# Optimization experiments

Hardware: AMD Instinct MI355X
Metric: run time of the kernel (lower is better)

Reference implementation:

```python
import jax, jax.numpy as jnp
import numpy as np

EPS = 1e-6


def ln_fwd(x, gamma, beta):
    # layernorm over last dim (biased variance), per TTT ln_fwd
    mu = x.mean(-1, keepdims=True)
    var = x.var(-1, keepdims=True)
    xh = (x - mu) * jax.lax.rsqrt(var + EPS)
    return gamma * xh + beta


def ln_fused_l2_bwd(x, l2_target, gamma, beta):
    # grad of 0.5*||LN(x) - target||^2 w.r.t. x, fused (per TTT ln_fused_l2_bwd)
    D = x.shape[-1]
    mu = x.mean(-1, keepdims=True)
    var = x.var(-1, keepdims=True)
    std = jnp.sqrt(var + EPS)
    xh = (x - mu) / std
    y = gamma * xh + beta
    gxh = (y - l2_target) * gamma
    z = (D * gxh - gxh.sum(-1, keepdims=True) - xh * (gxh * xh).sum(-1, keepdims=True)) / (D * std)
    return z


def setup_inputs() -> dict:
    key = jax.random.key(0)
    ks = jax.random.split(key, 5)
    B, nh, nmb, mbs, hd = 8, 8, 256, 16, 64
    XQ = jax.random.normal(ks[0], (B, nh, nmb, mbs, hd), jnp.float32)
    XK = jax.random.normal(ks[1], (B, nh, nmb, mbs, hd), jnp.float32)
    XV = jax.random.normal(ks[2], (B, nh, nmb, mbs, hd), jnp.float32)
    # eta = small positive per-token learning rates (ttt_base_lr/head_dim scale)
    eta = jax.random.uniform(ks[3], (B, nh, nmb, mbs, mbs), jnp.float32) * (1.0 / hd)
    W1 = jax.random.normal(ks[4], (nh, hd, hd), jnp.float32) * 0.02
    b1 = jnp.zeros((nh, 1, hd), jnp.float32)
    ln_weight = jnp.ones((nh * hd,), jnp.float32)
    ln_bias = jnp.zeros((nh * hd,), jnp.float32)
    return {"XQ": XQ, "XK": XK, "XV": XV, "eta": eta, "W1": W1, "b1": b1,
            "ln_weight": ln_weight, "ln_bias": ln_bias}


def reference(XQ, XK, XV, eta, W1, b1, ln_weight, ln_bias):
    B, nh, nmb, mbs, hd = XQ.shape
    lnw = ln_weight.reshape(nh, 1, hd)
    lnb = ln_bias.reshape(nh, 1, hd)
    W1_0 = jnp.broadcast_to(W1[None], (B, nh, hd, hd))
    b1_0 = jnp.broadcast_to(b1[None], (B, nh, 1, hd))
    tril = jnp.tril(jnp.ones((mbs, mbs), XQ.dtype))

    def step(carry, inp):
        W1s, b1s = carry               # [B,nh,hd,hd], [B,nh,1,hd]
        xq, xk, xv, et = inp           # [B,nh,mbs,hd] x3, [B,nh,mbs,mbs]
        Z1 = xk @ W1s + b1s
        g = ln_fused_l2_bwd(Z1, xv - xk, lnw, lnb)          # grad_l_wrt_Z1
        Attn1 = tril * (xq @ jnp.swapaxes(xk, -1, -2))      # causal QK^T
        b1_bar = b1s - (tril * et) @ g
        Z1_bar = xq @ W1s - (et * Attn1) @ g + b1_bar
        last_eta = et[..., -1, :, None]                     # [B,nh,mbs,1]
        W1_last = W1s - jnp.swapaxes(last_eta * xk, -1, -2) @ g
        b1_last = b1s - jnp.sum(last_eta * g, axis=-2, keepdims=True)
        out = xq + ln_fwd(Z1_bar, lnw, lnb)
        return (W1_last, b1_last), out

    xs = (jnp.moveaxis(XQ, 2, 0), jnp.moveaxis(XK, 2, 0),
          jnp.moveaxis(XV, 2, 0), jnp.moveaxis(eta, 2, 0))
    _, outs = jax.lax.scan(step, (W1_0, b1_0), xs)
    # outs: [nmb,B,nh,mbs,hd] -> [B,nmb,mbs,nh,hd] -> [B,L,width]
    return jnp.transpose(outs, (1, 0, 3, 2, 4)).reshape(B, nmb * mbs, nh * hd)
```

## Files before the change

kernel.cpp:

```cpp
#include <hip/hip_runtime.h>
#include <hip/hip_bf16.h>

typedef __attribute__((ext_vector_type(8))) short short8;
typedef __attribute__((ext_vector_type(4))) short short4_t;
typedef __attribute__((ext_vector_type(4))) float f32x4;

constexpr int MBS = 16, HD = 64, NMB = 256;

#define MFMA32(a, b, c) __builtin_amdgcn_mfma_f32_16x16x32_bf16(a, b, c, 0, 0, 0)

#if __has_builtin(__builtin_amdgcn_mfma_f32_16x16x16bf16_1k)
#define MFMA16(a, b, c) __builtin_amdgcn_mfma_f32_16x16x16bf16_1k(a, b, c, 0, 0, 0)
#else
__device__ inline f32x4 mfma16_asm(short4_t a, short4_t b, f32x4 c) {
    asm volatile("v_mfma_f32_16x16x16_bf16 %0, %1, %2, %0\n\ts_nop 7\n\ts_nop 7"
                 : "+v"(c) : "v"(a), "v"(b));
    return c;
}
#define MFMA16(a, b, c) mfma16_asm(a, b, c)
#endif

#define TR_READ(dst, addr, IMM) \
    asm volatile("ds_read_b64_tr_b16 %0, %1 offset:" IMM : "=&v"(dst) : "v"(addr) : "memory")

union U2S4 { unsigned u[2]; short4_t s; };
union FI { float f; int i; };

__device__ inline unsigned pkbf(float a, float b) {
    union { __hip_bfloat162 h; unsigned u; } c;
    c.h = __float22bfloat162_rn(make_float2(a, b));
    return c.u;
}
__device__ inline short bf16s(float x) { return (short)(pkbf(x, 0.f) & 0xffffu); }
__device__ inline float dpp16(float x) {
    FI v; v.f = x; FI t;
    t.i = __builtin_amdgcn_update_dpp(0, v.i, 0xB1, 0xf, 0xf, true);  v.f += t.f;
    t.i = __builtin_amdgcn_update_dpp(0, v.i, 0x4E, 0xf, 0xf, true);  v.f += t.f;
    t.i = __builtin_amdgcn_update_dpp(0, v.i, 0x124, 0xf, 0xf, true); v.f += t.f;
    t.i = __builtin_amdgcn_update_dpp(0, v.i, 0x128, 0xf, 0xf, true); v.f += t.f;
    return v.f;
}
__device__ inline void bar() {
    __builtin_amdgcn_sched_barrier(0);
    asm volatile("s_waitcnt lgkmcnt(0)" ::: "memory");
    __builtin_amdgcn_s_barrier();
    __builtin_amdgcn_sched_barrier(0);
}

__global__ __launch_bounds__(256) void ttt_scan(
    const float* __restrict__ gXQ, const float* __restrict__ gXK,
    const float* __restrict__ gXV, const float* __restrict__ gETA,
    const float* __restrict__ gW1, const float* __restrict__ gB1,
    const float* __restrict__ gLNW, const float* __restrict__ gLNB,
    float* __restrict__ gOUT)
{
    __shared__ __align__(16) short sWt[64 * 72];
    __shared__ __align__(16) short bxk[16 * 72];
    __shared__ __align__(16) short bxq[16 * 72];
    __shared__ __align__(16) short sGt[1024];
    __shared__ __align__(16) short sXKe[1024];
    __shared__ __align__(16) short sE[16 * 20];
    __shared__ __align__(16) float sZ1[16 * 68];
    __shared__ __align__(16) float sZb[16 * 68];
    __shared__ __align__(16) float sEta[2][256];

    const int t  = threadIdx.x;
    const int s  = t >> 4;
    const int dt = t & 15;
    const int lane = t & 63;
    const int w  = t >> 6;
    const int gq = lane >> 4;
    const int lc = lane & 15;
    const int bh = blockIdx.x, b = bh >> 3, h = bh & 7;

    const float* xqg = gXQ + (size_t)bh * (NMB * MBS * HD);
    const float* xkg = gXK + (size_t)bh * (NMB * MBS * HD);
    const float* xvg = gXV + (size_t)bh * (NMB * MBS * HD);
    const float* etg = gETA + (size_t)bh * (NMB * MBS * MBS);

    f32x4 Wacc[4];
#pragma unroll
    for (int ct = 0; ct < 4; ++ct) {
#pragma unroll
        for (int r = 0; r < 4; ++r)
            Wacc[ct][r] = gW1[h * 4096 + (16 * w + 4 * gq + r) * 64 + 16 * ct + lc];
        U2S4 wp;
        wp.u[0] = pkbf(Wacc[ct][0], Wacc[ct][1]);
        wp.u[1] = pkbf(Wacc[ct][2], Wacc[ct][3]);
        *(short4_t*)&sWt[(16 * ct + lc) * 72 + 16 * w + 4 * gq] = wp.s;
    }
    float b1v = gB1[h * 64 + 16 * w + lc];

    const float4 gam = *(const float4*)&gLNW[h * 64 + dt * 4];
    const float4 bet = *(const float4*)&gLNB[h * 64 + dt * 4];
    const float ga[4] = {gam.x, gam.y, gam.z, gam.w};
    const float ba[4] = {bet.x, bet.y, bet.z, bet.w};
    float c1a[4], gba[4];
    float sc1 = 0.f;
#pragma unroll
    for (int c = 0; c < 4; ++c) {
        c1a[c] = ga[c] * ga[c];
        gba[c] = ga[c] * ba[c];
        sc1 += c1a[c];
    }
    sc1 = dpp16(sc1);

    float4 pq = *(const float4*)&xqg[t * 4];
    float4 pk = *(const float4*)&xkg[t * 4];
    float4 pv = *(const float4*)&xvg[t * 4];
    float4 pe = make_float4(0.f, 0.f, 0.f, 0.f);
    if (t < 64) pe = *(const float4*)&etg[t * 4];

    { U2S4 u_; u_.u[0]=pkbf(pk.x,pk.y); u_.u[1]=pkbf(pk.z,pk.w);
      *(short4_t*)&bxk[s * 72 + dt * 4] = u_.s; }
    { U2S4 u_; u_.u[0]=pkbf(pq.x,pq.y); u_.u[1]=pkbf(pq.z,pq.w);
      *(short4_t*)&bxq[s * 72 + dt * 4] = u_.s; }
    if (t < 64) *(float4*)&sEta[0][t * 4] = pe;
    float t2c[4];
    {
        const float pva[4] = {pv.x, pv.y, pv.z, pv.w};
        const float pka_[4] = {pk.x, pk.y, pk.z, pk.w};
#pragma unroll
        for (int c = 0; c < 4; ++c)
            t2c[c] = fmaf(-ga[c], pva[c] - pka_[c], gba[c]);
    }
    float4 pkc = pk;
    float4 pq_out = pq;
    float4 pq_prev_out;

    __syncthreads();

#pragma unroll 1
    for (int m = 0; m < NMB; ++m) {
        const int p = m & 1;

        if (m + 1 < NMB) {
            const size_t o = (size_t)(m + 1) * (MBS * HD) + t * 4;
            pq = *(const float4*)&xqg[o];
            pk = *(const float4*)&xkg[o];
            pv = *(const float4*)&xvg[o];
            if (t < 64) pe = *(const float4*)&etg[(size_t)(m + 1) * (MBS * MBS) + t * 4];
        }

        f32x4 z1a; z1a[0]=b1v; z1a[1]=b1v; z1a[2]=b1v; z1a[3]=b1v;
        f32x4 zqa = z1a;
        const short8 ak0 = *(const short8*)&bxk[lc * 72 + gq * 8];
        const short8 ak1 = *(const short8*)&bxk[lc * 72 + gq * 8 + 32];
        const short8 aq0 = *(const short8*)&bxq[lc * 72 + gq * 8];
        const short8 aq1 = *(const short8*)&bxq[lc * 72 + gq * 8 + 32];
        const short8 bw0 = *(const short8*)&sWt[(16 * w + lc) * 72 + gq * 8];
        const short8 bw1 = *(const short8*)&sWt[(16 * w + lc) * 72 + gq * 8 + 32];
        z1a = MFMA32(ak0, bw0, z1a); z1a = MFMA32(ak1, bw1, z1a);
        zqa = MFMA32(aq0, bw0, zqa); zqa = MFMA32(aq1, bw1, zqa);
#pragma unroll
        for (int r = 0; r < 4; ++r) sZ1[(4 * gq + r) * 68 + 16 * w + lc] = z1a[r];

        if (w == 3) {
            f32x4 zz; zz[0]=0.f; zz[1]=0.f; zz[2]=0.f; zz[3]=0.f;
            zz = MFMA32(aq0, ak0, zz); zz = MFMA32(aq1, ak1, zz);
#pragma unroll
            for (int r = 0; r < 4; ++r) {
                const int row = 4 * gq + r;
                const float ev = sEta[p][row * 16 + lc];
                const float x = (lc <= row) ? -ev * (1.f + zz[r]) : 0.f;
                sE[row * 20 + lc] = bf16s(x);
            }
        }

        if (m > 0) {
            f32x4 zbr = *(f32x4*)&sZb[s * 68 + dt * 4];
            float T1 = 0.f, T2 = 0.f;
#pragma unroll
            for (int c = 0; c < 4; ++c) { T1 += zbr[c]; T2 = fmaf(zbr[c], zbr[c], T2); }
            T1 = dpp16(T1); T2 = dpp16(T2);
            const float mu2   = T1 * (1.f / 64.f);
            const float rstd2 = rsqrtf(T2 * (1.f / 64.f) - mu2 * mu2 + 1e-6f);
            const float pqa[4] = {pq_prev_out.x, pq_prev_out.y, pq_prev_out.z, pq_prev_out.w};
            float o[4];
#pragma unroll
            for (int c = 0; c < 4; ++c)
                o[c] = pqa[c] + fmaf(ga[c], (zbr[c] - mu2) * rstd2, ba[c]);
            const size_t oi = ((size_t)b * 4096 + (size_t)(m - 1) * 16 + s) * 512 + h * 64 + dt * 4;
            *(float4*)&gOUT[oi] = make_float4(o[0], o[1], o[2], o[3]);
        }
        bar();

        f32x4 z = *(f32x4*)&sZ1[s * 68 + dt * 4];
        float S1=0.f,S2=0.f,S3=0.f,S4=0.f,S5=0.f,S6=0.f;
#pragma unroll
        for (int c = 0; c < 4; ++c) {
            const float zc = z[c], c1z = c1a[c] * zc, t2 = t2c[c];
            S1 += zc;  S2 = fmaf(zc, zc, S2);
            S3 += c1z; S4 = fmaf(c1z, zc, S4);
            S5 += t2;  S6 = fmaf(t2, zc, S6);
        }
        S1 = dpp16(S1); S2 = dpp16(S2); S3 = dpp16(S3);
        S4 = dpp16(S4); S5 = dpp16(S5); S6 = dpp16(S6);
        const float mu   = S1 * (1.f / 64.f);
        const float rstd = rsqrtf(S2 * (1.f / 64.f) - mu * mu + 1e-6f);
        const float r1 = rstd * (S3 - mu * sc1) + S5;
        const float r2 = rstd * rstd * (S4 - 2.f * mu * S3 + mu * mu * sc1)
                       + rstd * (S6 - mu * S5);
        const float cf = rstd * (1.f / 64.f);
        float g[4];
#pragma unroll
        for (int c = 0; c < 4; ++c) {
            const float xh = (z[c] - mu) * rstd;
            const float gx = fmaf(c1a[c], xh, t2c[c]);
            g[c] = (fmaf(64.f, gx, -r1) - xh * r2) * cf;
        }

        const float le = sEta[p][240 + s];
        const int tb = (s >> 2) * 256 + (dt >> 2) * 64 + (s & 3) * 16 + (dt & 3) * 4;
        { U2S4 gp; gp.u[0]=pkbf(g[0],g[1]); gp.u[1]=pkbf(g[2],g[3]);
          *(short4_t*)&sGt[tb] = gp.s; }
        { U2S4 kp; kp.u[0]=pkbf(-le*pkc.x,-le*pkc.y); kp.u[1]=pkbf(-le*pkc.z,-le*pkc.w);
          *(short4_t*)&sXKe[tb] = kp.s; }
        bar();

        const unsigned gbase = (unsigned)(size_t)&sGt[0] + 512u * gq + 8u * lc;
        const unsigned kbase = (unsigned)(size_t)&sXKe[0] + 512u * gq + 128u * (unsigned)w + 8u * lc;
        short4_t bg0, bg1, bg2, bg3, aK;
        TR_READ(bg0, gbase, "0");
        TR_READ(bg1, gbase, "128");
        TR_READ(bg2, gbase, "256");
        TR_READ(bg3, gbase, "384");
        TR_READ(aK,  kbase, "0");
        const short4_t aE = *(const short4_t*)&sE[lc * 20 + gq * 4];
        const f32x4 lv = *(const f32x4*)&sEta[p][240 + 4 * gq];
        U2S4 aL;
        aL.u[0] = pkbf(-lv[0], -lv[1]);
        aL.u[1] = pkbf(-lv[2], -lv[3]);
        asm volatile("s_waitcnt lgkmcnt(0)" ::: "memory");
        __builtin_amdgcn_sched_barrier(0);

        short4_t bgw = bg0;
        if (w == 1) bgw = bg1;
        else if (w == 2) bgw = bg2;
        else if (w == 3) bgw = bg3;

        f32x4 zb = MFMA16(aE, bgw, zqa);
#pragma unroll
        for (int r = 0; r < 4; ++r) sZb[(4 * gq + r) * 68 + 16 * w + lc] = zb[r];

        Wacc[0] = MFMA16(aK, bg0, Wacc[0]);
        Wacc[1] = MFMA16(aK, bg1, Wacc[1]);
        Wacc[2] = MFMA16(aK, bg2, Wacc[2]);
        Wacc[3] = MFMA16(aK, bg3, Wacc[3]);
        {
            f32x4 d0; d0[0]=0.f; d0[1]=0.f; d0[2]=0.f; d0[3]=0.f;
            d0 = MFMA16(aL.s, bgw, d0);
            b1v += d0[0];
        }
#pragma unroll
        for (int ct = 0; ct < 4; ++ct) {
            U2S4 wp;
            wp.u[0] = pkbf(Wacc[ct][0], Wacc[ct][1]);
            wp.u[1] = pkbf(Wacc[ct][2], Wacc[ct][3]);
            *(short4_t*)&sWt[(16 * ct + lc) * 72 + 16 * w + 4 * gq] = wp.s;
        }

        if (m + 1 < NMB) {
            { U2S4 u_; u_.u[0]=pkbf(pk.x,pk.y); u_.u[1]=pkbf(pk.z,pk.w);
              *(short4_t*)&bxk[s * 72 + dt * 4] = u_.s; }
            { U2S4 u_; u_.u[0]=pkbf(pq.x,pq.y); u_.u[1]=pkbf(pq.z,pq.w);
              *(short4_t*)&bxq[s * 72 + dt * 4] = u_.s; }
            if (t < 64) *(float4*)&sEta[p ^ 1][t * 4] = pe;
#pragma unroll
            for (int c = 0; c < 4; ++c) {
                const float pva[4] = {pv.x, pv.y, pv.z, pv.w};
                const float pka_[4] = {pk.x, pk.y, pk.z, pk.w};
                t2c[c] = fmaf(-ga[c], pva[c] - pka_[c], gba[c]);
            }
            pkc = pk;
        }
        pq_prev_out = pq_out;
        pq_out = pq;
        bar();
    }

    {
        f32x4 zbr = *(f32x4*)&sZb[s * 68 + dt * 4];
        float T1 = 0.f, T2 = 0.f;
#pragma unroll
        for (int c = 0; c < 4; ++c) { T1 += zbr[c]; T2 = fmaf(zbr[c], zbr[c], T2); }
        T1 = dpp16(T1); T2 = dpp16(T2);
        const float mu2   = T1 * (1.f / 64.f);
        const float rstd2 = rsqrtf(T2 * (1.f / 64.f) - mu2 * mu2 + 1e-6f);
        const float pqa[4] = {pq_prev_out.x, pq_prev_out.y, pq_prev_out.z, pq_prev_out.w};
        float o[4];
#pragma unroll
        for (int c = 0; c < 4; ++c)
            o[c] = pqa[c] + fmaf(ga[c], (zbr[c] - mu2) * rstd2, ba[c]);
        const size_t oi = ((size_t)b * 4096 + (size_t)(NMB - 1) * 16 + s) * 512 + h * 64 + dt * 4;
        *(float4*)&gOUT[oi] = make_float4(o[0], o[1], o[2], o[3]);
    }
}

extern "C" void kernel_launch(void* const* d_in, const int* in_sizes, int n_in,
                              void* d_out, int out_size, void* d_ws, size_t ws_size,
                              hipStream_t stream) {
    const float* XQ  = (const float*)d_in[0];
    const float* XK  = (const float*)d_in[1];
    const float* XV  = (const float*)d_in[2];
    const float* ETA = (const float*)d_in[3];
    const float* W1  = (const float*)d_in[4];
    const float* B1  = (const float*)d_in[5];
    const float* LNW = (const float*)d_in[6];
    const float* LNB = (const float*)d_in[7];
    float* OUT = (float*)d_out;

    const int n_chains = in_sizes[0] / (NMB * MBS * HD);
    ttt_scan<<<n_chains, 256, 0, stream>>>(XQ, XK, XV, ETA, W1, B1, LNW, LNB, OUT);
}
```

Before: 374.7 us.

## Run each TTT chain in a single wavefront with register-resident W

```diff
diff --git a/kernel.cpp b/kernel.cpp
--- a/kernel.cpp
+++ b/kernel.cpp
@@ -1,13 +1,10 @@
 #include <hip/hip_runtime.h>
 #include <hip/hip_bf16.h>
 
-typedef __attribute__((ext_vector_type(8))) short short8;
 typedef __attribute__((ext_vector_type(4))) short short4_t;
 typedef __attribute__((ext_vector_type(4))) float f32x4;
 
-constexpr int MBS = 16, HD = 64, NMB = 256;
-
-#define MFMA32(a, b, c) __builtin_amdgcn_mfma_f32_16x16x32_bf16(a, b, c, 0, 0, 0)
+constexpr int NMB = 256;
 
 #if __has_builtin(__builtin_amdgcn_mfma_f32_16x16x16bf16_1k)
 #define MFMA16(a, b, c) __builtin_amdgcn_mfma_f32_16x16x16bf16_1k(a, b, c, 0, 0, 0)
@@ -32,6 +29,9 @@
     return c.u;
 }
 __device__ inline short bf16s(float x) { return (short)(pkbf(x, 0.f) & 0xffffu); }
+__device__ inline short4_t pk4(float a, float b, float c, float d) {
+    U2S4 u; u.u[0] = pkbf(a, b); u.u[1] = pkbf(c, d); return u.s;
+}
 __device__ inline float dpp16(float x) {
     FI v; v.f = x; FI t;
     t.i = __builtin_amdgcn_update_dpp(0, v.i, 0xB1, 0xf, 0xf, true);  v.f += t.f;
@@ -40,260 +40,245 @@
     t.i = __builtin_amdgcn_update_dpp(0, v.i, 0x128, 0xf, 0xf, true); v.f += t.f;
     return v.f;
 }
-__device__ inline void bar() {
-    __builtin_amdgcn_sched_barrier(0);
-    asm volatile("s_waitcnt lgkmcnt(0)" ::: "memory");
-    __builtin_amdgcn_s_barrier();
-    __builtin_amdgcn_sched_barrier(0);
-}
-
-__global__ __launch_bounds__(256) void ttt_scan(
+
+__global__ __launch_bounds__(64) void ttt_scan(
     const float* __restrict__ gXQ, const float* __restrict__ gXK,
     const float* __restrict__ gXV, const float* __restrict__ gETA,
     const float* __restrict__ gW1, const float* __restrict__ gB1,
     const float* __restrict__ gLNW, const float* __restrict__ gLNB,
     float* __restrict__ gOUT)
 {
-    __shared__ __align__(16) short sWt[64 * 72];
-    __shared__ __align__(16) short bxk[16 * 72];
-    __shared__ __align__(16) short bxq[16 * 72];
-    __shared__ __align__(16) short sGt[1024];
     __shared__ __align__(16) short sXKe[1024];
     __shared__ __align__(16) short sE[16 * 20];
-    __shared__ __align__(16) float sZ1[16 * 68];
-    __shared__ __align__(16) float sZb[16 * 68];
     __shared__ __align__(16) float sEta[2][256];
 
-    const int t  = threadIdx.x;
-    const int s  = t >> 4;
-    const int dt = t & 15;
-    const int lane = t & 63;
-    const int w  = t >> 6;
-    const int gq = lane >> 4;
-    const int lc = lane & 15;
+    const int l = threadIdx.x;
+    const int G = l >> 4, l15 = l & 15;
     const int bh = blockIdx.x, b = bh >> 3, h = bh & 7;
 
-    const float* xqg = gXQ + (size_t)bh * (NMB * MBS * HD);
-    const float* xkg = gXK + (size_t)bh * (NMB * MBS * HD);
-    const float* xvg = gXV + (size_t)bh * (NMB * MBS * HD);
-    const float* etg = gETA + (size_t)bh * (NMB * MBS * MBS);
-
-    f32x4 Wacc[4];
-#pragma unroll
-    for (int ct = 0; ct < 4; ++ct) {
-#pragma unroll
-        for (int r = 0; r < 4; ++r)
-            Wacc[ct][r] = gW1[h * 4096 + (16 * w + 4 * gq + r) * 64 + 16 * ct + lc];
-        U2S4 wp;
-        wp.u[0] = pkbf(Wacc[ct][0], Wacc[ct][1]);
-        wp.u[1] = pkbf(Wacc[ct][2], Wacc[ct][3]);
-        *(short4_t*)&sWt[(16 * ct + lc) * 72 + 16 * w + 4 * gq] = wp.s;
-    }
-    float b1v = gB1[h * 64 + 16 * w + lc];
-
-    const float4 gam = *(const float4*)&gLNW[h * 64 + dt * 4];
-    const float4 bet = *(const float4*)&gLNB[h * 64 + dt * 4];
-    const float ga[4] = {gam.x, gam.y, gam.z, gam.w};
-    const float ba[4] = {bet.x, bet.y, bet.z, bet.w};
-    float c1a[4], gba[4];
-    float sc1 = 0.f;
-#pragma unroll
-    for (int c = 0; c < 4; ++c) {
-        c1a[c] = ga[c] * ga[c];
-        gba[c] = ga[c] * ba[c];
-        sc1 += c1a[c];
-    }
-    sc1 = dpp16(sc1);
-
-    float4 pq = *(const float4*)&xqg[t * 4];
-    float4 pk = *(const float4*)&xkg[t * 4];
-    float4 pv = *(const float4*)&xvg[t * 4];
-    float4 pe = make_float4(0.f, 0.f, 0.f, 0.f);
-    if (t < 64) pe = *(const float4*)&etg[t * 4];
-
-    { U2S4 u_; u_.u[0]=pkbf(pk.x,pk.y); u_.u[1]=pkbf(pk.z,pk.w);
-      *(short4_t*)&bxk[s * 72 + dt * 4] = u_.s; }
-    { U2S4 u_; u_.u[0]=pkbf(pq.x,pq.y); u_.u[1]=pkbf(pq.z,pq.w);
-      *(short4_t*)&bxq[s * 72 + dt * 4] = u_.s; }
-    if (t < 64) *(float4*)&sEta[0][t * 4] = pe;
-    float t2c[4];
+    const float* xqg = gXQ + (size_t)bh * (NMB * 1024);
+    const float* xkg = gXK + (size_t)bh * (NMB * 1024);
+    const float* xvg = gXV + (size_t)bh * (NMB * 1024);
+    const float* etg = gETA + (size_t)bh * (NMB * 256);
+
+    float gaC[4], betC[4], c1C[4], gbC[4];
+#pragma unroll
+    for (int nt = 0; nt < 4; ++nt) {
+        gaC[nt]  = gLNW[h * 64 + 16 * nt + l15];
+        betC[nt] = gLNB[h * 64 + 16 * nt + l15];
+        c1C[nt]  = gaC[nt] * gaC[nt];
+        gbC[nt]  = gaC[nt] * betC[nt];
+    }
+    const float sc1 = dpp16(c1C[0] + c1C[1] + c1C[2] + c1C[3]);
+
+    f32x4 Wacc[4][4];
+    short4_t WB[4][4];
+#pragma unroll
+    for (int kt = 0; kt < 4; ++kt)
+#pragma unroll
+        for (int nt = 0; nt < 4; ++nt) {
+#pragma unroll
+            for (int r = 0; r < 4; ++r)
+                Wacc[kt][nt][r] = gW1[h * 4096 + (16 * kt + 4 * G + r) * 64 + 16 * nt + l15];
+            WB[kt][nt] = pk4(Wacc[kt][nt][0], Wacc[kt][nt][1], Wacc[kt][nt][2], Wacc[kt][nt][3]);
+        }
+    f32x4 b1v;
+#pragma unroll
+    for (int nt = 0; nt < 4; ++nt) b1v[nt] = gB1[h * 64 + 16 * nt + l15];
+
+    U2S4 ones_;
+    ones_.u[0] = 0x3F803F80u; ones_.u[1] = 0x3F803F80u;
+    const short4_t onesA = ones_.s;
+
+    short4_t ak[4], aq[4];
+#pragma unroll
+    for (int kt = 0; kt < 4; ++kt) {
+        const f32x4 fk = *(const f32x4*)&xkg[l15 * 64 + 16 * kt + 4 * G];
+        const f32x4 fq = *(const f32x4*)&xqg[l15 * 64 + 16 * kt + 4 * G];
+        ak[kt] = pk4(fk[0], fk[1], fk[2], fk[3]);
+        aq[kt] = pk4(fq[0], fq[1], fq[2], fq[3]);
+    }
+#pragma unroll
+    for (int kt = 0; kt < 4; ++kt)
+        *(short4_t*)&sXKe[(l15 >> 2) * 256 + kt * 64 + (l15 & 3) * 16 + 4 * G] = ak[kt];
+    float xkC[4][4], xvC[4][4], xqC[4][4];
+#pragma unroll
+    for (int r = 0; r < 4; ++r)
+#pragma unroll
+        for (int nt = 0; nt < 4; ++nt) {
+            xkC[r][nt] = xkg[(4 * G + r) * 64 + 16 * nt + l15];
+            xvC[r][nt] = xvg[(4 * G + r) * 64 + 16 * nt + l15];
+            xqC[r][nt] = xqg[(4 * G + r) * 64 + 16 * nt + l15];
+        }
     {
-        const float pva[4] = {pv.x, pv.y, pv.z, pv.w};
-        const float pka_[4] = {pk.x, pk.y, pk.z, pk.w};
-#pragma unroll
-        for (int c = 0; c < 4; ++c)
-            t2c[c] = fmaf(-ga[c], pva[c] - pka_[c], gba[c]);
-    }
-    float4 pkc = pk;
-    float4 pq_out = pq;
-    float4 pq_prev_out;
-
-    __syncthreads();
+        const f32x4 e0 = *(const f32x4*)&etg[l * 4];
+        *(f32x4*)&sEta[0][l * 4] = e0;
+    }
+    f32x4 etaF = *(const f32x4*)&etg[256 + l * 4];
+    f32x4 fkn[4], fqn[4];
+#pragma unroll
+    for (int kt = 0; kt < 4; ++kt) {
+        fkn[kt] = *(const f32x4*)&xkg[1024 + l15 * 64 + 16 * kt + 4 * G];
+        fqn[kt] = *(const f32x4*)&xqg[1024 + l15 * 64 + 16 * kt + 4 * G];
+    }
 
 #pragma unroll 1
     for (int m = 0; m < NMB; ++m) {
         const int p = m & 1;
 
+        f32x4 z1[4], zq[4];
+#pragma unroll
+        for (int nt = 0; nt < 4; ++nt) {
+            f32x4 c0; c0[0] = b1v[nt]; c0[1] = b1v[nt]; c0[2] = b1v[nt]; c0[3] = b1v[nt];
+            f32x4 a_ = c0, q_ = c0;
+#pragma unroll
+            for (int kt = 0; kt < 4; ++kt) a_ = MFMA16(ak[kt], WB[kt][nt], a_);
+#pragma unroll
+            for (int kt = 0; kt < 4; ++kt) q_ = MFMA16(aq[kt], WB[kt][nt], q_);
+            z1[nt] = a_; zq[nt] = q_;
+        }
+        f32x4 at; at[0] = 0.f; at[1] = 0.f; at[2] = 0.f; at[3] = 0.f;
+#pragma unroll
+        for (int kt = 0; kt < 4; ++kt) at = MFMA16(aq[kt], ak[kt], at);
+
+        const f32x4 lef = *(const f32x4*)&sEta[p][240 + 4 * G];
+        float mu[4], rs[4];
+#pragma unroll
+        for (int r = 0; r < 4; ++r) {
+            const float s1 = dpp16(z1[0][r] + z1[1][r] + z1[2][r] + z1[3][r]);
+            const float s2 = dpp16(z1[0][r]*z1[0][r] + z1[1][r]*z1[1][r]
+                                 + z1[2][r]*z1[2][r] + z1[3][r]*z1[3][r]);
+            mu[r] = s1 * (1.f / 64.f);
+            rs[r] = rsqrtf(s2 * (1.f / 64.f) - mu[r] * mu[r] + 1e-6f);
+        }
+        float gx[4][4], r1[4], r2[4];
+#pragma unroll
+        for (int r = 0; r < 4; ++r) {
+            float p1 = 0.f, p2 = 0.f;
+#pragma unroll
+            for (int nt = 0; nt < 4; ++nt) {
+                const float xh = (z1[nt][r] - mu[r]) * rs[r];
+                const float t2 = gbC[nt] - gaC[nt] * (xvC[r][nt] - xkC[r][nt]);
+                const float gg = fmaf(c1C[nt], xh, t2);
+                gx[r][nt] = gg;
+                p1 += gg; p2 = fmaf(gg, xh, p2);
+            }
+            r1[r] = dpp16(p1); r2[r] = dpp16(p2);
+        }
+        float gt[4][4];
+#pragma unroll
+        for (int r = 0; r < 4; ++r) {
+            const float cf = rs[r] * (1.f / 64.f);
+#pragma unroll
+            for (int nt = 0; nt < 4; ++nt) {
+                const float xh = (z1[nt][r] - mu[r]) * rs[r];
+                gt[r][nt] = (fmaf(64.f, gx[r][nt], -r1[r]) - xh * r2[r]) * cf;
+            }
+        }
+        short4_t g_b[4], gle_b[4];
+#pragma unroll
+        for (int nt = 0; nt < 4; ++nt) {
+            g_b[nt]   = pk4(gt[0][nt], gt[1][nt], gt[2][nt], gt[3][nt]);
+            gle_b[nt] = pk4(-lef[0] * gt[0][nt], -lef[1] * gt[1][nt],
+                            -lef[2] * gt[2][nt], -lef[3] * gt[3][nt]);
+        }
+
         if (m + 1 < NMB) {
-            const size_t o = (size_t)(m + 1) * (MBS * HD) + t * 4;
-            pq = *(const float4*)&xqg[o];
-            pk = *(const float4*)&xkg[o];
-            pv = *(const float4*)&xvg[o];
-            if (t < 64) pe = *(const float4*)&etg[(size_t)(m + 1) * (MBS * MBS) + t * 4];
-        }
-
-        f32x4 z1a; z1a[0]=b1v; z1a[1]=b1v; z1a[2]=b1v; z1a[3]=b1v;
-        f32x4 zqa = z1a;
-        const short8 ak0 = *(const short8*)&bxk[lc * 72 + gq * 8];
-        const short8 ak1 = *(const short8*)&bxk[lc * 72 + gq * 8 + 32];
-        const short8 aq0 = *(const short8*)&bxq[lc * 72 + gq * 8];
-        const short8 aq1 = *(const short8*)&bxq[lc * 72 + gq * 8 + 32];
-        const short8 bw0 = *(const short8*)&sWt[(16 * w + lc) * 72 + gq * 8];
-        const short8 bw1 = *(const short8*)&sWt[(16 * w + lc) * 72 + gq * 8 + 32];
-        z1a = MFMA32(ak0, bw0, z1a); z1a = MFMA32(ak1, bw1, z1a);
-        zqa = MFMA32(aq0, bw0, zqa); zqa = MFMA32(aq1, bw1, zqa);
-#pragma unroll
-        for (int r = 0; r < 4; ++r) sZ1[(4 * gq + r) * 68 + 16 * w + lc] = z1a[r];
-
-        if (w == 3) {
-            f32x4 zz; zz[0]=0.f; zz[1]=0.f; zz[2]=0.f; zz[3]=0.f;
-            zz = MFMA32(aq0, ak0, zz); zz = MFMA32(aq1, ak1, zz);
-#pragma unroll
-            for (int r = 0; r < 4; ++r) {
-                const int row = 4 * gq + r;
-                const float ev = sEta[p][row * 16 + lc];
-                const float x = (lc <= row) ? -ev * (1.f + zz[r]) : 0.f;
-                sE[row * 20 + lc] = bf16s(x);
-            }
-        }
-
-        if (m > 0) {
-            f32x4 zbr = *(f32x4*)&sZb[s * 68 + dt * 4];
-            float T1 = 0.f, T2 = 0.f;
-#pragma unroll
-            for (int c = 0; c < 4; ++c) { T1 += zbr[c]; T2 = fmaf(zbr[c], zbr[c], T2); }
-            T1 = dpp16(T1); T2 = dpp16(T2);
-            const float mu2   = T1 * (1.f / 64.f);
-            const float rstd2 = rsqrtf(T2 * (1.f / 64.f) - mu2 * mu2 + 1e-6f);
-            const float pqa[4] = {pq_prev_out.x, pq_prev_out.y, pq_prev_out.z, pq_prev_out.w};
-            float o[4];
-#pragma unroll
-            for (int c = 0; c < 4; ++c)
-                o[c] = pqa[c] + fmaf(ga[c], (zbr[c] - mu2) * rstd2, ba[c]);
-            const size_t oi = ((size_t)b * 4096 + (size_t)(m - 1) * 16 + s) * 512 + h * 64 + dt * 4;
-            *(float4*)&gOUT[oi] = make_float4(o[0], o[1], o[2], o[3]);
-        }
-        bar();
-
-        f32x4 z = *(f32x4*)&sZ1[s * 68 + dt * 4];
-        float S1=0.f,S2=0.f,S3=0.f,S4=0.f,S5=0.f,S6=0.f;
-#pragma unroll
-        for (int c = 0; c < 4; ++c) {
-            const float zc = z[c], c1z = c1a[c] * zc, t2 = t2c[c];
-            S1 += zc;  S2 = fmaf(zc, zc, S2);
-            S3 += c1z; S4 = fmaf(c1z, zc, S4);
-            S5 += t2;  S6 = fmaf(t2, zc, S6);
-        }
-        S1 = dpp16(S1); S2 = dpp16(S2); S3 = dpp16(S3);
-        S4 = dpp16(S4); S5 = dpp16(S5); S6 = dpp16(S6);
-        const float mu   = S1 * (1.f / 64.f);
-        const float rstd = rsqrtf(S2 * (1.f / 64.f) - mu * mu + 1e-6f);
-        const float r1 = rstd * (S3 - mu * sc1) + S5;
-        const float r2 = rstd * rstd * (S4 - 2.f * mu * S3 + mu * mu * sc1)
-                       + rstd * (S6 - mu * S5);
-        const float cf = rstd * (1.f / 64.f);
-        float g[4];
-#pragma unroll
-        for (int c = 0; c < 4; ++c) {
-            const float xh = (z[c] - mu) * rstd;
-            const float gx = fmaf(c1a[c], xh, t2c[c]);
-            g[c] = (fmaf(64.f, gx, -r1) - xh * r2) * cf;
-        }
-
-        const float le = sEta[p][240 + s];
-        const int tb = (s >> 2) * 256 + (dt >> 2) * 64 + (s & 3) * 16 + (dt & 3) * 4;
-        { U2S4 gp; gp.u[0]=pkbf(g[0],g[1]); gp.u[1]=pkbf(g[2],g[3]);
-          *(short4_t*)&sGt[tb] = gp.s; }
-        { U2S4 kp; kp.u[0]=pkbf(-le*pkc.x,-le*pkc.y); kp.u[1]=pkbf(-le*pkc.z,-le*pkc.w);
-          *(short4_t*)&sXKe[tb] = kp.s; }
-        bar();
-
-        const unsigned gbase = (unsigned)(size_t)&sGt[0] + 512u * gq + 8u * lc;
-        const unsigned kbase = (unsigned)(size_t)&sXKe[0] + 512u * gq + 128u * (unsigned)w + 8u * lc;
-        short4_t bg0, bg1, bg2, bg3, aK;
-        TR_READ(bg0, gbase, "0");
-        TR_READ(bg1, gbase, "128");
-        TR_READ(bg2, gbase, "256");
-        TR_READ(bg3, gbase, "384");
-        TR_READ(aK,  kbase, "0");
-        const short4_t aE = *(const short4_t*)&sE[lc * 20 + gq * 4];
-        const f32x4 lv = *(const f32x4*)&sEta[p][240 + 4 * gq];
-        U2S4 aL;
-        aL.u[0] = pkbf(-lv[0], -lv[1]);
-        aL.u[1] = pkbf(-lv[2], -lv[3]);
+            const size_t o = (size_t)(m + 1) * 1024;
+#pragma unroll
+            for (int r = 0; r < 4; ++r)
+#pragma unroll
+                for (int nt = 0; nt < 4; ++nt) {
+                    xkC[r][nt] = xkg[o + (4 * G + r) * 64 + 16 * nt + l15];
+                    xvC[r][nt] = xvg[o + (4 * G + r) * 64 + 16 * nt + l15];
+                }
+        }
+
+#pragma unroll
+        for (int r = 0; r < 4; ++r) {
+            const float ev = sEta[p][(4 * G + r) * 16 + l15];
+            const float e = (l15 <= 4 * G + r) ? -ev * (1.f + at[r]) : 0.f;
+            sE[(4 * G + r) * 20 + l15] = bf16s(e);
+        }
         asm volatile("s_waitcnt lgkmcnt(0)" ::: "memory");
         __builtin_amdgcn_sched_barrier(0);
 
-        short4_t bgw = bg0;
-        if (w == 1) bgw = bg1;
-        else if (w == 2) bgw = bg2;
-        else if (w == 3) bgw = bg3;
-
-        f32x4 zb = MFMA16(aE, bgw, zqa);
-#pragma unroll
-        for (int r = 0; r < 4; ++r) sZb[(4 * gq + r) * 68 + 16 * w + lc] = zb[r];
-
-        Wacc[0] = MFMA16(aK, bg0, Wacc[0]);
-        Wacc[1] = MFMA16(aK, bg1, Wacc[1]);
-        Wacc[2] = MFMA16(aK, bg2, Wacc[2]);
-        Wacc[3] = MFMA16(aK, bg3, Wacc[3]);
-        {
-            f32x4 d0; d0[0]=0.f; d0[1]=0.f; d0[2]=0.f; d0[3]=0.f;
-            d0 = MFMA16(aL.s, bgw, d0);
-            b1v += d0[0];
-        }
-#pragma unroll
-        for (int ct = 0; ct < 4; ++ct) {
-            U2S4 wp;
-            wp.u[0] = pkbf(Wacc[ct][0], Wacc[ct][1]);
-            wp.u[1] = pkbf(Wacc[ct][2], Wacc[ct][3]);
-            *(short4_t*)&sWt[(16 * ct + lc) * 72 + 16 * w + 4 * gq] = wp.s;
-        }
-
+        const unsigned kb = (unsigned)(size_t)&sXKe[0] + 512u * G + 8u * l15;
+        short4_t aXK0, aXK1, aXK2, aXK3;
+        TR_READ(aXK0, kb, "0");
+        TR_READ(aXK1, kb, "128");
+        TR_READ(aXK2, kb, "256");
+        TR_READ(aXK3, kb, "384");
+        const short4_t aE = *(const short4_t*)&sE[l15 * 20 + 4 * G];
+        asm volatile("s_waitcnt lgkmcnt(0)" ::: "memory");
+        __builtin_amdgcn_sched_barrier(0);
+
+#pragma unroll
+        for (int nt = 0; nt < 4; ++nt) {
+            Wacc[0][nt] = MFMA16(aXK0, gle_b[nt], Wacc[0][nt]);
+            Wacc[1][nt] = MFMA16(aXK1, gle_b[nt], Wacc[1][nt]);
+            Wacc[2][nt] = MFMA16(aXK2, gle_b[nt], Wacc[2][nt]);
+            Wacc[3][nt] = MFMA16(aXK3, gle_b[nt], Wacc[3][nt]);
+        }
+        f32x4 zb[4];
+#pragma unroll
+        for (int nt = 0; nt < 4; ++nt) {
+            zb[nt] = MFMA16(aE, g_b[nt], zq[nt]);
+            f32x4 d0; d0[0] = 0.f; d0[1] = 0.f; d0[2] = 0.f; d0[3] = 0.f;
+            d0 = MFMA16(onesA, gle_b[nt], d0);
+            b1v[nt] += d0[0];
+        }
+#pragma unroll
+        for (int kt = 0; kt < 4; ++kt)
+#pragma unroll
+            for (int nt = 0; nt < 4; ++nt)
+                WB[kt][nt] = pk4(Wacc[kt][nt][0], Wacc[kt][nt][1],
+                                 Wacc[kt][nt][2], Wacc[kt][nt][3]);
+
+        float mu2[4], rs2[4];
+#pragma unroll
+        for (int r = 0; r < 4; ++r) {
+            const float t1 = dpp16(zb[0][r] + zb[1][r] + zb[2][r] + zb[3][r]);
+            const float t2 = dpp16(zb[0][r]*zb[0][r] + zb[1][r]*zb[1][r]
+                                 + zb[2][r]*zb[2][r] + zb[3][r]*zb[3][r]);
+            mu2[r] = t1 * (1.f / 64.f);
+            rs2[r] = rsqrtf(t2 * (1.f / 64.f) - mu2[r] * mu2[r] + 1e-6f);
+        }
+#pragma unroll
+        for (int r = 0; r < 4; ++r) {
+            const size_t ob = ((size_t)b * 4096 + (size_t)m * 16 + 4 * G + r) * 512 + h * 64 + l15;
+#pragma unroll
+            for (int nt = 0; nt < 4; ++nt)
+                gOUT[ob + 16 * nt] =
+                    xqC[r][nt] + fmaf(gaC[nt], (zb[nt][r] - mu2[r]) * rs2[r], betC[nt]);
+        }
         if (m + 1 < NMB) {
-            { U2S4 u_; u_.u[0]=pkbf(pk.x,pk.y); u_.u[1]=pkbf(pk.z,pk.w);
-              *(short4_t*)&bxk[s * 72 + dt * 4] = u_.s; }
-            { U2S4 u_; u_.u[0]=pkbf(pq.x,pq.y); u_.u[1]=pkbf(pq.z,pq.w);
-              *(short4_t*)&bxq[s * 72 + dt * 4] = u_.s; }
-            if (t < 64) *(float4*)&sEta[p ^ 1][t * 4] = pe;
-#pragma unroll
-            for (int c = 0; c < 4; ++c) {
-                const float pva[4] = {pv.x, pv.y, pv.z, pv.w};
-                const float pka_[4] = {pk.x, pk.y, pk.z, pk.w};
-                t2c[c] = fmaf(-ga[c], pva[c] - pka_[c], gba[c]);
+            const size_t o = (size_t)(m + 1) * 1024;
+#pragma unroll
+            for (int r = 0; r < 4; ++r)
+#pragma unroll
+                for (int nt = 0; nt < 4; ++nt)
+                    xqC[r][nt] = xqg[o + (4 * G + r) * 64 + 16 * nt + l15];
+        }
+
+        if (m + 1 < NMB) {
+#pragma unroll
+            for (int kt = 0; kt < 4; ++kt) {
+                ak[kt] = pk4(fkn[kt][0], fkn[kt][1], fkn[kt][2], fkn[kt][3]);
+                aq[kt] = pk4(fqn[kt][0], fqn[kt][1], fqn[kt][2], fqn[kt][3]);
+                *(short4_t*)&sXKe[(l15 >> 2) * 256 + kt * 64 + (l15 & 3) * 16 + 4 * G] = ak[kt];
             }
-            pkc = pk;
-        }
-        pq_prev_out = pq_out;
-        pq_out = pq;
-        bar();
-    }
-
-    {
-        f32x4 zbr = *(f32x4*)&sZb[s * 68 + dt * 4];
-        float T1 = 0.f, T2 = 0.f;
-#pragma unroll
-        for (int c = 0; c < 4; ++c) { T1 += zbr[c]; T2 = fmaf(zbr[c], zbr[c], T2); }
-        T1 = dpp16(T1); T2 = dpp16(T2);
-        const float mu2   = T1 * (1.f / 64.f);
-        const float rstd2 = rsqrtf(T2 * (1.f / 64.f) - mu2 * mu2 + 1e-6f);
-        const float pqa[4] = {pq_prev_out.x, pq_prev_out.y, pq_prev_out.z, pq_prev_out.w};
-        float o[4];
-#pragma unroll
-        for (int c = 0; c < 4; ++c)
-            o[c] = pqa[c] + fmaf(ga[c], (zbr[c] - mu2) * rstd2, ba[c]);
-        const size_t oi = ((size_t)b * 4096 + (size_t)(NMB - 1) * 16 + s) * 512 + h * 64 + dt * 4;
-        *(float4*)&gOUT[oi] = make_float4(o[0], o[1], o[2], o[3]);
+            *(f32x4*)&sEta[p ^ 1][l * 4] = etaF;
+            if (m + 2 < NMB) {
+                const size_t o2 = (size_t)(m + 2) * 1024;
+#pragma unroll
+                for (int kt = 0; kt < 4; ++kt) {
+                    fkn[kt] = *(const f32x4*)&xkg[o2 + l15 * 64 + 16 * kt + 4 * G];
+                    fqn[kt] = *(const f32x4*)&xqg[o2 + l15 * 64 + 16 * kt + 4 * G];
+                }
+                etaF = *(const f32x4*)&etg[(size_t)(m + 2) * 256 + l * 4];
+            }
+        }
     }
 }
 
@@ -310,6 +295,6 @@
     const float* LNB = (const float*)d_in[7];
     float* OUT = (float*)d_out;
 
-    const int n_chains = in_sizes[0] / (NMB * MBS * HD);
-    ttt_scan<<<n_chains, 256, 0, stream>>>(XQ, XK, XV, ETA, W1, B1, LNW, LNB, OUT);
-}
+    const int n_chains = in_sizes[0] / (NMB * 1024);
+    ttt_scan<<<n_chains, 64, 0, stream>>>(XQ, XK, XV, ETA, W1, B1, LNW, LNB, OUT);
+}
```

After: 793.3 us. +111.7%, slower.

## Keep W1 and XK/XQ MFMA operands in registers instead of shared memory

Applied to the files above, without the earlier changes.

```diff
diff --git a/kernel.cpp b/kernel.cpp
--- a/kernel.cpp
+++ b/kernel.cpp
@@ -1,13 +1,10 @@
 #include <hip/hip_runtime.h>
 #include <hip/hip_bf16.h>
 
-typedef __attribute__((ext_vector_type(8))) short short8;
 typedef __attribute__((ext_vector_type(4))) short short4_t;
 typedef __attribute__((ext_vector_type(4))) float f32x4;
 
-constexpr int MBS = 16, HD = 64, NMB = 256;
-
-#define MFMA32(a, b, c) __builtin_amdgcn_mfma_f32_16x16x32_bf16(a, b, c, 0, 0, 0)
+constexpr int NMB = 256;
 
 #if __has_builtin(__builtin_amdgcn_mfma_f32_16x16x16bf16_1k)
 #define MFMA16(a, b, c) __builtin_amdgcn_mfma_f32_16x16x16bf16_1k(a, b, c, 0, 0, 0)
@@ -32,6 +29,9 @@
     return c.u;
 }
 __device__ inline short bf16s(float x) { return (short)(pkbf(x, 0.f) & 0xffffu); }
+__device__ inline short4_t pk4(float a, float b, float c, float d) {
+    U2S4 u; u.u[0] = pkbf(a, b); u.u[1] = pkbf(c, d); return u.s;
+}
 __device__ inline float dpp16(float x) {
     FI v; v.f = x; FI t;
     t.i = __builtin_amdgcn_update_dpp(0, v.i, 0xB1, 0xf, 0xf, true);  v.f += t.f;
@@ -54,9 +54,6 @@
     const float* __restrict__ gLNW, const float* __restrict__ gLNB,
     float* __restrict__ gOUT)
 {
-    __shared__ __align__(16) short sWt[64 * 72];
-    __shared__ __align__(16) short bxk[16 * 72];
-    __shared__ __align__(16) short bxq[16 * 72];
     __shared__ __align__(16) short sGt[1024];
     __shared__ __align__(16) short sXKe[1024];
     __shared__ __align__(16) short sE[16 * 20];
@@ -69,27 +66,24 @@
     const int dt = t & 15;
     const int lane = t & 63;
     const int w  = t >> 6;
-    const int gq = lane >> 4;
-    const int lc = lane & 15;
+    const int G  = lane >> 4;
+    const int l15 = lane & 15;
     const int bh = blockIdx.x, b = bh >> 3, h = bh & 7;
 
-    const float* xqg = gXQ + (size_t)bh * (NMB * MBS * HD);
-    const float* xkg = gXK + (size_t)bh * (NMB * MBS * HD);
-    const float* xvg = gXV + (size_t)bh * (NMB * MBS * HD);
-    const float* etg = gETA + (size_t)bh * (NMB * MBS * MBS);
-
-    f32x4 Wacc[4];
-#pragma unroll
-    for (int ct = 0; ct < 4; ++ct) {
+    const float* xqg = gXQ + (size_t)bh * (NMB * 1024);
+    const float* xkg = gXK + (size_t)bh * (NMB * 1024);
+    const float* xvg = gXV + (size_t)bh * (NMB * 1024);
+    const float* etg = gETA + (size_t)bh * (NMB * 256);
+
+    f32x4 Wacc[4]; short4_t WB[4];
+#pragma unroll
+    for (int kt = 0; kt < 4; ++kt) {
 #pragma unroll
         for (int r = 0; r < 4; ++r)
-            Wacc[ct][r] = gW1[h * 4096 + (16 * w + 4 * gq + r) * 64 + 16 * ct + lc];
-        U2S4 wp;
-        wp.u[0] = pkbf(Wacc[ct][0], Wacc[ct][1]);
-        wp.u[1] = pkbf(Wacc[ct][2], Wacc[ct][3]);
-        *(short4_t*)&sWt[(16 * ct + lc) * 72 + 16 * w + 4 * gq] = wp.s;
-    }
-    float b1v = gB1[h * 64 + 16 * w + lc];
+            Wacc[kt][r] = gW1[h * 4096 + (16 * kt + 4 * G + r) * 64 + 16 * w + l15];
+        WB[kt] = pk4(Wacc[kt][0], Wacc[kt][1], Wacc[kt][2], Wacc[kt][3]);
+    }
+    float b1v = gB1[h * 64 + 16 * w + l15];
 
     const float4 gam = *(const float4*)&gLNW[h * 64 + dt * 4];
     const float4 bet = *(const float4*)&gLNB[h * 64 + dt * 4];
@@ -110,12 +104,18 @@
     float4 pv = *(const float4*)&xvg[t * 4];
     float4 pe = make_float4(0.f, 0.f, 0.f, 0.f);
     if (t < 64) pe = *(const float4*)&etg[t * 4];
-
-    { U2S4 u_; u_.u[0]=pkbf(pk.x,pk.y); u_.u[1]=pkbf(pk.z,pk.w);
-      *(short4_t*)&bxk[s * 72 + dt * 4] = u_.s; }
-    { U2S4 u_; u_.u[0]=pkbf(pq.x,pq.y); u_.u[1]=pkbf(pq.z,pq.w);
-      *(short4_t*)&bxq[s * 72 + dt * 4] = u_.s; }
     if (t < 64) *(float4*)&sEta[0][t * 4] = pe;
+
+    short4_t ak[4], aq[4];
+#pragma unroll
+    for (int kt = 0; kt < 4; ++kt) {
+        const f32x4 fk = *(const f32x4*)&xkg[l15 * 64 + 16 * kt + 4 * G];
+        const f32x4 fq = *(const f32x4*)&xqg[l15 * 64 + 16 * kt + 4 * G];
+        ak[kt] = pk4(fk[0], fk[1], fk[2], fk[3]);
+        aq[kt] = pk4(fq[0], fq[1], fq[2], fq[3]);
+    }
+    f32x4 fkn[4], fqn[4];
+
     float t2c[4];
     {
         const float pva[4] = {pv.x, pv.y, pv.z, pv.w};
@@ -135,35 +135,39 @@
         const int p = m & 1;
 
         if (m + 1 < NMB) {
-            const size_t o = (size_t)(m + 1) * (MBS * HD) + t * 4;
+            const size_t o = (size_t)(m + 1) * 1024 + t * 4;
             pq = *(const float4*)&xqg[o];
             pk = *(const float4*)&xkg[o];
             pv = *(const float4*)&xvg[o];
-            if (t < 64) pe = *(const float4*)&etg[(size_t)(m + 1) * (MBS * MBS) + t * 4];
-        }
-
-        f32x4 z1a; z1a[0]=b1v; z1a[1]=b1v; z1a[2]=b1v; z1a[3]=b1v;
-        f32x4 zqa = z1a;
-        const short8 ak0 = *(const short8*)&bxk[lc * 72 + gq * 8];
-        const short8 ak1 = *(const short8*)&bxk[lc * 72 + gq * 8 + 32];
-        const short8 aq0 = *(const short8*)&bxq[lc * 72 + gq * 8];
-        const short8 aq1 = *(const short8*)&bxq[lc * 72 + gq * 8 + 32];
-        const short8 bw0 = *(const short8*)&sWt[(16 * w + lc) * 72 + gq * 8];
-        const short8 bw1 = *(const short8*)&sWt[(16 * w + lc) * 72 + gq * 8 + 32];
-        z1a = MFMA32(ak0, bw0, z1a); z1a = MFMA32(ak1, bw1, z1a);
-        zqa = MFMA32(aq0, bw0, zqa); zqa = MFMA32(aq1, bw1, zqa);
-#pragma unroll
-        for (int r = 0; r < 4; ++r) sZ1[(4 * gq + r) * 68 + 16 * w + lc] = z1a[r];
+            if (t < 64) pe = *(const float4*)&etg[(size_t)(m + 1) * 256 + t * 4];
+            const size_t ow = (size_t)(m + 1) * 1024 + l15 * 64 + 4 * G;
+#pragma unroll
+            for (int kt = 0; kt < 4; ++kt) {
+                fkn[kt] = *(const f32x4*)&xkg[ow + 16 * kt];
+                fqn[kt] = *(const f32x4*)&xqg[ow + 16 * kt];
+            }
+        }
+
+        f32x4 z1, zq;
+        z1[0]=b1v; z1[1]=b1v; z1[2]=b1v; z1[3]=b1v;
+        zq = z1;
+#pragma unroll
+        for (int kt = 0; kt < 4; ++kt) z1 = MFMA16(ak[kt], WB[kt], z1);
+#pragma unroll
+        for (int kt = 0; kt < 4; ++kt) zq = MFMA16(aq[kt], WB[kt], zq);
+#pragma unroll
+        for (int r = 0; r < 4; ++r) sZ1[(4 * G + r) * 68 + 16 * w + l15] = z1[r];
 
         if (w == 3) {
-            f32x4 zz; zz[0]=0.f; zz[1]=0.f; zz[2]=0.f; zz[3]=0.f;
-            zz = MFMA32(aq0, ak0, zz); zz = MFMA32(aq1, ak1, zz);
+            f32x4 at; at[0]=0.f; at[1]=0.f; at[2]=0.f; at[3]=0.f;
+#pragma unroll
+            for (int kt = 0; kt < 4; ++kt) at = MFMA16(aq[kt], ak[kt], at);
 #pragma unroll
             for (int r = 0; r < 4; ++r) {
-                const int row = 4 * gq + r;
-                const float ev = sEta[p][row * 16 + lc];
-                const float x = (lc <= row) ? -ev * (1.f + zz[r]) : 0.f;
-                sE[row * 20 + lc] = bf16s(x);
+                const int row = 4 * G + r;
+                const float ev = sEta[p][row * 16 + l15];
+                const float x = (l15 <= row) ? -ev * (1.f + at[r]) : 0.f;
+                sE[row * 20 + l15] = bf16s(x);
             }
         }
 
@@ -209,7 +213,6 @@
             const float gx = fmaf(c1a[c], xh, t2c[c]);
             g[c] = (fmaf(64.f, gx, -r1) - xh * r2) * cf;
         }
-
         const float le = sEta[p][240 + s];
         const int tb = (s >> 2) * 256 + (dt >> 2) * 64 + (s & 3) * 16 + (dt & 3) * 4;
         { U2S4 gp; gp.u[0]=pkbf(g[0],g[1]); gp.u[1]=pkbf(g[2],g[3]);
@@ -218,53 +221,44 @@
           *(short4_t*)&sXKe[tb] = kp.s; }
         bar();
 
-        const unsigned gbase = (unsigned)(size_t)&sGt[0] + 512u * gq + 8u * lc;
-        const unsigned kbase = (unsigned)(size_t)&sXKe[0] + 512u * gq + 128u * (unsigned)w + 8u * lc;
-        short4_t bg0, bg1, bg2, bg3, aK;
-        TR_READ(bg0, gbase, "0");
-        TR_READ(bg1, gbase, "128");
-        TR_READ(bg2, gbase, "256");
-        TR_READ(bg3, gbase, "384");
-        TR_READ(aK,  kbase, "0");
-        const short4_t aE = *(const short4_t*)&sE[lc * 20 + gq * 4];
-        const f32x4 lv = *(const f32x4*)&sEta[p][240 + 4 * gq];
+        const unsigned kbX = (unsigned)(size_t)&sXKe[0] + 512u * G + 8u * l15;
+        const unsigned kbG = (unsigned)(size_t)&sGt[0] + 512u * G + 128u * (unsigned)w + 8u * l15;
+        short4_t aXK0, aXK1, aXK2, aXK3, bg;
+        TR_READ(aXK0, kbX, "0");
+        TR_READ(aXK1, kbX, "128");
+        TR_READ(aXK2, kbX, "256");
+        TR_READ(aXK3, kbX, "384");
+        TR_READ(bg,   kbG, "0");
+        const short4_t aE = *(const short4_t*)&sE[l15 * 20 + 4 * G];
+        const f32x4 lv = *(const f32x4*)&sEta[p][240 + 4 * G];
         U2S4 aL;
         aL.u[0] = pkbf(-lv[0], -lv[1]);
         aL.u[1] = pkbf(-lv[2], -lv[3]);
         asm volatile("s_waitcnt lgkmcnt(0)" ::: "memory");
         __builtin_amdgcn_sched_barrier(0);
 
-        short4_t bgw = bg0;
-        if (w == 1) bgw = bg1;
-        else if (w == 2) bgw = bg2;
-        else if (w == 3) bgw = bg3;
-
-        f32x4 zb = MFMA16(aE, bgw, zqa);
-#pragma unroll
-        for (int r = 0; r < 4; ++r) sZb[(4 * gq + r) * 68 + 16 * w + lc] = zb[r];
-
-        Wacc[0] = MFMA16(aK, bg0, Wacc[0]);
-        Wacc[1] = MFMA16(aK, bg1, Wacc[1]);
-        Wacc[2] = MFMA16(aK, bg2, Wacc[2]);
-        Wacc[3] = MFMA16(aK, bg3, Wacc[3]);
+        Wacc[0] = MFMA16(aXK0, bg, Wacc[0]);
+        Wacc[1] = MFMA16(aXK1, bg, Wacc[1]);
+        Wacc[2] = MFMA16(aXK2, bg, Wacc[2]);
+        Wacc[3] = MFMA16(aXK3, bg, Wacc[3]);
+        f32x4 zb = MFMA16(aE, bg, zq);
         {
             f32x4 d0; d0[0]=0.f; d0[1]=0.f; d0[2]=0.f; d0[3]=0.f;
-            d0 = MFMA16(aL.s, bgw, d0);
+            d0 = MFMA16(aL.s, bg, d0);
             b1v += d0[0];
         }
 #pragma unroll
-        for (int ct = 0; ct < 4; ++ct) {
-            U2S4 wp;
-            wp.u[0] = pkbf(Wacc[ct][0], Wacc[ct][1]);
-            wp.u[1] = pkbf(Wacc[ct][2], Wacc[ct][3]);
-            *(short4_t*)&sWt[(16 * ct + lc) * 72 + 16 * w + 4 * gq] = wp.s;
-        }
+        for (int kt = 0; kt < 4; ++kt)
+            WB[kt] = pk4(Wacc[kt][0], Wacc[kt][1], Wacc[kt][2], Wacc[kt][3]);
+#pragma unroll
+        for (int r = 0; r < 4; ++r) sZb[(4 * G + r) * 68 + 16 * w + l15] = zb[r];
 
         if (m + 1 < NMB) {
-            { U2S4 u_; u_.u[0]=pkbf(pk.x,pk.y); u_.u[1]=pkbf(pk.z,pk.w);
-              *(short4_t*)&bxk[s * 72 + dt * 4] = u_.s; }
-            { U2S4 u_; u_.u[0]=pkbf(pq.x,pq.y); u_.u[1]=pkbf(pq.z,pq.w);
-              *(short4_t*)&bxq[s * 72 + dt * 4] = u_.s; }
+#pragma unroll
+            for (int kt = 0; kt < 4; ++kt) {
+                ak[kt] = pk4(fkn[kt][0], fkn[kt][1], fkn[kt][2], fkn[kt][3]);
+                aq[kt] = pk4(fqn[kt][0], fqn[kt][1], fqn[kt][2], fqn[kt][3]);
+            }
             if (t < 64) *(float4*)&sEta[p ^ 1][t * 4] = pe;
 #pragma unroll
             for (int c = 0; c < 4; ++c) {
@@ -310,6 +304,6 @@
     const float* LNB = (const float*)d_in[7];
     float* OUT = (float*)d_out;
 
-    const int n_chains = in_sizes[0] / (NMB * MBS * HD);
+    const int n_chains = in_sizes[0] / (NMB * 1024);
     ttt_scan<<<n_chains, 256, 0, stream>>>(XQ, XK, XV, ETA, W1, B1, LNW, LNB, OUT);
 }
```

Result: slower. 454.2 us (+21.2%).
